# Kernel optimization log

Measured on AMD Instinct MI355X. Metric: run time of the kernel, lower is better.

The kernel has to match this reference:

```python
import jax, jax.numpy as jnp
import numpy as np

N = 100000      # nodes
E = 1600000     # edges
FX = 128        # raw node feature dim
MAXZ = 100      # z embedding / one-hot size
HID = 128       # hidden_channels
NL = 3          # num_layers
G = 512         # num graphs
BN_EPS = 1e-5


def _lin(key, din, dout):
    return jax.random.normal(key, (din, dout), jnp.float32) * (1.0 / np.sqrt(din))


def setup_inputs() -> dict:
    key = jax.random.key(0)
    ks = jax.random.split(key, 64)
    d = {}
    d["x"] = jax.random.normal(ks[0], (N, FX), jnp.float32)
    d["z"] = jax.random.randint(ks[1], (N,), 0, MAXZ)
    d["edge_index"] = jax.random.randint(ks[2], (2, E), 0, N)
    d["batch"] = jnp.sort(jax.random.randint(ks[3], (N,), 0, G))
    in0 = FX + 2 * MAXZ  # z_emb concatenated twice (faithful to source)
    ki = 4
    for l in range(NL):
        din = in0 if l == 0 else HID
        d[f"W1_{l}"] = _lin(ks[ki], din, HID); ki += 1
        d[f"b1_{l}"] = jnp.zeros((HID,), jnp.float32)
        d[f"W2_{l}"] = _lin(ks[ki], HID, HID); ki += 1
        d[f"b2_{l}"] = jnp.zeros((HID,), jnp.float32)
        d[f"g_{l}"] = jnp.ones((HID,), jnp.float32)
        d[f"be_{l}"] = jnp.zeros((HID,), jnp.float32)
    d["Wl1"] = _lin(ks[ki], NL * HID, HID); ki += 1
    d["bl1"] = jnp.zeros((HID,), jnp.float32)
    d["Wl2"] = _lin(ks[ki], HID, 1); ki += 1
    d["bl2"] = jnp.zeros((1,), jnp.float32)
    return d


def _gin_layer(h, src, dst, W1, b1, W2, b2, g, be):
    # GINConv with eps=0: nn(x + sum_{j->i} x_j)
    agg = jax.ops.segment_sum(h[src], dst, num_segments=N)  # [N, d]
    m = h + agg
    m = jax.nn.relu(m @ W1 + b1)
    m = jax.nn.relu(m @ W2 + b2)
    # training-mode BatchNorm1d over node axis (biased variance)
    mu = m.mean(0)
    var = jnp.mean((m - mu) ** 2, axis=0)
    return (m - mu) * jax.lax.rsqrt(var + BN_EPS) * g + be


def reference(x, z, edge_index, batch,
              W1_0, b1_0, W2_0, b2_0, g_0, be_0,
              W1_1, b1_1, W2_1, b2_1, g_1, be_1,
              W1_2, b1_2, W2_2, b2_2, g_2, be_2,
              Wl1, bl1, Wl2, bl2):
    src, dst = edge_index[0], edge_index[1]
    z_emb = jax.nn.one_hot(z, MAXZ, dtype=jnp.float32)  # [N, MAXZ]
    h = jnp.concatenate([z_emb, x], axis=1)
    h = jnp.concatenate([z_emb, h], axis=1)  # faithful double concat -> [N, FX+2*MAXZ]
    params = [(W1_0, b1_0, W2_0, b2_0, g_0, be_0),
              (W1_1, b1_1, W2_1, b2_1, g_1, be_1),
              (W1_2, b1_2, W2_2, b2_2, g_2, be_2)]
    xs = []
    for p in params:
        h = _gin_layer(h, src, dst, *p)
        xs.append(h)
    hcat = jnp.concatenate(xs, axis=1)  # jumping knowledge: [N, NL*HID]
    # global_mean_pool over graph ids
    counts = jax.ops.segment_sum(jnp.ones((N,), jnp.float32), batch, num_segments=G)
    pooled = jax.ops.segment_sum(hcat, batch, num_segments=G) / jnp.maximum(counts, 1.0)[:, None]
    out = jax.nn.relu(pooled @ Wl1 + bl1)
    # dropout is identity in eval / reference mode
    out = out @ Wl2 + bl2  # [G, 1]
    return out
```

## Files before the change

kernel.cpp:

```cpp
#include <hip/hip_runtime.h>
#include <hip/hip_bf16.h>

#define NN 100000
#define NROWS_PAD 100032
#define EE 1600000
#define GG 512
#define SCAN_CHUNK 512
#define SCAN_BLOCKS ((NN + SCAN_CHUNK - 1) / SCAN_CHUNK)
#define NPB 256
#define NB  ((NN + NPB - 1) / NPB)
#define PCHUNK 4096
#define PBLOCKS ((EE + PCHUNK - 1) / PCHUNK)
static constexpr float BN_EPS = 1e-5f;

typedef _Float16 half8 __attribute__((ext_vector_type(8)));
typedef _Float16 half4 __attribute__((ext_vector_type(4)));
typedef float floatx4 __attribute__((ext_vector_type(4)));


__global__ __launch_bounds__(256) void k_bhist(const int* __restrict__ EI,
                                               int* __restrict__ bcount)
{
    __shared__ int h[NB];
    const int t = threadIdx.x;
    for (int i = t; i < NB; i += 256) h[i] = 0;
    __syncthreads();
    const int e0 = blockIdx.x * PCHUNK;
    const int e1 = (e0 + PCHUNK < EE) ? e0 + PCHUNK : EE;
    for (int e = e0 + t; e < e1; e += 256)
        atomicAdd(&h[EI[EE + e] >> 8], 1);
    __syncthreads();
    for (int i = t; i < NB; i += 256)
        if (h[i]) atomicAdd(&bcount[i], h[i]);
}

__global__ __launch_bounds__(512) void k_bscan(const int* __restrict__ bcount,
                                               int* __restrict__ bstart,
                                               int* __restrict__ bcursor)
{
    __shared__ int s[512];
    int t = threadIdx.x;
    int v = (t < NB) ? bcount[t] : 0;
    s[t] = v;
    __syncthreads();
    for (int off = 1; off < 512; off <<= 1) {
        int u = (t >= off) ? s[t - off] : 0;
        __syncthreads();
        s[t] += u;
        __syncthreads();
    }
    if (t < NB) { int ex = s[t] - v; bstart[t] = ex; bcursor[t] = ex; }
    if (t == 0) bstart[NB] = EE;
}

__global__ __launch_bounds__(256) void k_part(const int* __restrict__ EI,
                                              int* __restrict__ bcursor,
                                              int* __restrict__ ebuf)
{
    __shared__ int h[NB];
    __shared__ int cur[NB];
    const int t = threadIdx.x;
    for (int i = t; i < NB; i += 256) h[i] = 0;
    __syncthreads();
    const int e0 = blockIdx.x * PCHUNK;
    const int e1 = (e0 + PCHUNK < EE) ? e0 + PCHUNK : EE;
    for (int e = e0 + t; e < e1; e += 256)
        atomicAdd(&h[EI[EE + e] >> 8], 1);
    __syncthreads();
    for (int i = t; i < NB; i += 256)
        cur[i] = h[i] ? atomicAdd(&bcursor[i], h[i]) : 0;
    __syncthreads();
    for (int e = e0 + t; e < e1; e += 256) {
        int s = EI[e], d = EI[EE + e];
        int pos = atomicAdd(&cur[d >> 8], 1);
        ebuf[pos] = s | ((d & (NPB - 1)) << 17);
    }
}

__global__ __launch_bounds__(256) void k_nhist(const int* __restrict__ ebuf,
                                               const int* __restrict__ bstart,
                                               int* __restrict__ hist)
{
    __shared__ int cnt[NPB];
    const int b = blockIdx.x, t = threadIdx.x;
    cnt[t] = 0;
    __syncthreads();
    const int e0 = bstart[b], e1 = bstart[b + 1];
    for (int e = e0 + t; e < e1; e += 256) {
        unsigned p = (unsigned)__builtin_nontemporal_load(&ebuf[e]);
        atomicAdd(&cnt[p >> 17], 1);
    }
    __syncthreads();
    int idx = b * NPB + t;
    if (idx < NN) hist[idx] = cnt[t];
}

__global__ __launch_bounds__(256) void k_scan1(const int* __restrict__ hist,
                                               int* __restrict__ partials)
{
    __shared__ int red[256];
    int b = blockIdx.x, t = threadIdx.x;
    int i0 = b * SCAN_CHUNK + 2 * t;
    int e0 = (i0 < NN) ? hist[i0] : 0;
    int e1 = (i0 + 1 < NN) ? hist[i0 + 1] : 0;
    red[t] = e0 + e1;
    __syncthreads();
    for (int off = 128; off > 0; off >>= 1) {
        if (t < off) red[t] += red[t + off];
        __syncthreads();
    }
    if (t == 0) partials[b] = red[0];
}

__global__ __launch_bounds__(256) void k_scan2(const int* __restrict__ partials,
                                               int* __restrict__ poffs,
                                               int* __restrict__ row_start)
{
    __shared__ int s[256];
    int t = threadIdx.x;
    int v = (t < SCAN_BLOCKS) ? partials[t] : 0;
    s[t] = v;
    __syncthreads();
    for (int off = 1; off < 256; off <<= 1) {
        int u = (t >= off) ? s[t - off] : 0;
        __syncthreads();
        s[t] += u;
        __syncthreads();
    }
    if (t < SCAN_BLOCKS) poffs[t] = s[t] - v;
    if (t == 0) row_start[NN] = EE;
}

__global__ __launch_bounds__(256) void k_scan3(const int* __restrict__ hist,
                                               const int* __restrict__ poffs,
                                               int* __restrict__ row_start)
{
    __shared__ int s[256];
    int b = blockIdx.x, t = threadIdx.x;
    int i0 = b * SCAN_CHUNK + 2 * t;
    int e0 = (i0 < NN) ? hist[i0] : 0;
    int e1 = (i0 + 1 < NN) ? hist[i0 + 1] : 0;
    int pair = e0 + e1;
    s[t] = pair;
    __syncthreads();
    for (int off = 1; off < 256; off <<= 1) {
        int u = (t >= off) ? s[t - off] : 0;
        __syncthreads();
        s[t] += u;
        __syncthreads();
    }
    int base = poffs[b] + s[t] - pair;
    if (i0 < NN)     row_start[i0] = base;
    if (i0 + 1 < NN) row_start[i0 + 1] = base + e0;
}

__global__ __launch_bounds__(256) void k_fill2(const int* __restrict__ ebuf,
                                               const int* __restrict__ bstart,
                                               const int* __restrict__ row_start,
                                               int* __restrict__ ssrc)
{
    __shared__ int cur[NPB];
    const int b = blockIdx.x, t = threadIdx.x;
    int idx = b * NPB + t;
    cur[t] = (idx < NN) ? row_start[idx] : 0;
    __syncthreads();
    const int e0 = bstart[b], e1 = bstart[b + 1];
    for (int e = e0 + t; e < e1; e += 256) {
        unsigned p = (unsigned)__builtin_nontemporal_load(&ebuf[e]);
        int pos = atomicAdd(&cur[p >> 17], 1);
        ssrc[pos] = (int)(p & 0x1FFFFu);
    }
}


__global__ __launch_bounds__(256) void k_xcast(const float* __restrict__ X,
                                               _Float16* __restrict__ Xh)
{
    int idx = blockIdx.x * 256 + threadIdx.x;
    const float4* src = (const float4*)X;
    float4 a = src[idx * 2], b = src[idx * 2 + 1];
    half8 o = { (_Float16)a.x, (_Float16)a.y, (_Float16)a.z, (_Float16)a.w,
                (_Float16)b.x, (_Float16)b.y, (_Float16)b.z, (_Float16)b.w };
    *(half8*)&Xh[idx * 8] = o;
}

__global__ __launch_bounds__(256) void k_prep(
    const float* __restrict__ W1, const float* __restrict__ W2,
    const float* __restrict__ scale, const float* __restrict__ shift,
    _Float16* __restrict__ Wt1, _Float16* __restrict__ Wt2,
    float* __restrict__ cvec, int l)
{
    int b = blockIdx.x, t = threadIdx.x;
    if (b < 64) {
        int idx = b * 256 + t;
        int n = idx >> 7, k = idx & 127;
        Wt1[idx] = (l == 0) ? (_Float16)W1[(200 + k) * 128 + n]
                            : (_Float16)(scale[k] * W1[k * 128 + n]);
    } else if (b < 128) {
        int idx = (b - 64) * 256 + t;
        int n = idx >> 7, k = idx & 127;
        Wt2[idx] = (_Float16)W2[k * 128 + n];
    } else if (t < 128) {
        float acc = 0.f;
        if (l != 0)
            for (int k = 0; k < 128; ++k) acc = fmaf(shift[k], W1[k * 128 + t], acc);
        cvec[t] = acc;
    }
}


#define MM_PREAMBLE(Wth)                                                     \
    __shared__ _Float16 Wl[128][136];                                        \
    const int tid = threadIdx.x;                                             \
    const int row0 = blockIdx.x * 64;                                        \
    {                                                                        \
        for (int it = 0; it < 8; ++it) {                                     \
            int idx = tid + it * 256;                                        \
            int r = idx >> 4, seg = idx & 15;                                \
            *(half8*)&Wl[r][seg * 8] = *(const half8*)&Wth[r * 128 + seg * 8];\
        }                                                                    \
    }

#define MM_CORE(Ah)                                                          \
    const int lane = tid & 63;                                               \
    const int wv = tid >> 6;                                                 \
    const int ml = lane & 15;                                                \
    const int quad = lane >> 4;                                              \
    const int wr = wv >> 1, wc = wv & 1;                                     \
    floatx4 acc[2][4];                                                       \
    for (int r = 0; r < 2; ++r)                                              \
        for (int t = 0; t < 4; ++t)                                          \
            acc[r][t] = (floatx4){0.f, 0.f, 0.f, 0.f};                       \
    {                                                                        \
        const size_t ar0 = (size_t)(row0 + 32 * wr + ml) * 128;              \
        const size_t ar1 = ar0 + (size_t)16 * 128;                           \
        _Pragma("unroll")                                                    \
        for (int kq = 0; kq < 4; ++kq) {                                     \
            int k0 = kq * 32;                                                \
            half8 a0 = *(const half8*)&Ah[ar0 + k0 + quad * 8];              \
            half8 a1 = *(const half8*)&Ah[ar1 + k0 + quad * 8];              \
            _Pragma("unroll")                                                \
            for (int t = 0; t < 4; ++t) {                                    \
                half8 bf = *(const half8*)&Wl[64 * wc + 16 * t + ml][k0 + quad * 8]; \
                acc[0][t] = __builtin_amdgcn_mfma_f32_16x16x32_f16(a0, bf, acc[0][t], 0, 0, 0); \
                acc[1][t] = __builtin_amdgcn_mfma_f32_16x16x32_f16(a1, bf, acc[1][t], 0, 0, 0); \
            }                                                                \
        }                                                                    \
    }

__global__ __launch_bounds__(256) void k_mm_embed(
    const _Float16* __restrict__ Ah, const _Float16* __restrict__ Wth,
    const int* __restrict__ Z, const float* __restrict__ W1,
    _Float16* __restrict__ Ph)
{
    MM_PREAMBLE(Wth)
    __syncthreads();
    MM_CORE(Ah)
    #pragma unroll
    for (int r = 0; r < 2; ++r)
        #pragma unroll
        for (int j = 0; j < 4; ++j) {
            int grow = row0 + 32 * wr + 16 * r + quad * 4 + j;
            if (grow < NN) {
                int zv = Z[grow];
                const float* w0 = &W1[zv * 128];
                const float* w1 = &W1[(100 + zv) * 128];
                #pragma unroll
                for (int t = 0; t < 4; ++t) {
                    int gcol = 64 * wc + 16 * t + ml;
                    float v = acc[r][t][j] + w0[gcol] + w1[gcol];
                    Ph[(size_t)grow * 128 + gcol] = (_Float16)v;
                }
            }
        }
}

__global__ __launch_bounds__(256) void k_mm1(
    const _Float16* __restrict__ Ah, const _Float16* __restrict__ Wth,
    _Float16* __restrict__ Ph)
{
    MM_PREAMBLE(Wth)
    __syncthreads();
    MM_CORE(Ah)
    #pragma unroll
    for (int r = 0; r < 2; ++r)
        #pragma unroll
        for (int j = 0; j < 4; ++j) {
            int grow = row0 + 32 * wr + 16 * r + quad * 4 + j;
            if (grow < NN) {
                #pragma unroll
                for (int t = 0; t < 4; ++t) {
                    int gcol = 64 * wc + 16 * t + ml;
                    Ph[(size_t)grow * 128 + gcol] = (_Float16)acc[r][t][j];
                }
            }
        }
}

__global__ __launch_bounds__(256) void k_mm2(
    const _Float16* __restrict__ Ah, const _Float16* __restrict__ Wth,
    const float* __restrict__ b2, _Float16* __restrict__ Oh,
    float* __restrict__ colsum, float* __restrict__ colsq)
{
    __shared__ float cs[128];
    __shared__ float cq[128];
    MM_PREAMBLE(Wth)
    if (tid < 128) { cs[tid] = 0.f; cq[tid] = 0.f; }
    __syncthreads();
    MM_CORE(Ah)
    float b2v[4];
    #pragma unroll
    for (int t = 0; t < 4; ++t) b2v[t] = b2[64 * wc + 16 * t + ml];
    float st[4] = {0.f, 0.f, 0.f, 0.f};
    float qt[4] = {0.f, 0.f, 0.f, 0.f};
    #pragma unroll
    for (int r = 0; r < 2; ++r)
        #pragma unroll
        for (int j = 0; j < 4; ++j) {
            int grow = row0 + 32 * wr + 16 * r + quad * 4 + j;
            if (grow < NN) {
                #pragma unroll
                for (int t = 0; t < 4; ++t) {
                    int gcol = 64 * wc + 16 * t + ml;
                    float v = fmaxf(acc[r][t][j] + b2v[t], 0.f);
                    Oh[(size_t)grow * 128 + gcol] = (_Float16)v;
                    st[t] += v;
                    qt[t] += v * v;
                }
            }
        }
    #pragma unroll
    for (int t = 0; t < 4; ++t) {
        int gcol = 64 * wc + 16 * t + ml;
        atomicAdd(&cs[gcol], st[t]);
        atomicAdd(&cq[gcol], qt[t]);
    }
    __syncthreads();
    if (tid < 128) {
        atomicAdd(&colsum[tid], cs[tid]);
        atomicAdd(&colsq[tid], cq[tid]);
    }
}


__global__ __launch_bounds__(256) void k_aggregate(
    const _Float16* __restrict__ Ph, const int* __restrict__ row_start,
    const int* __restrict__ ssrc, const float* __restrict__ b1,
    const float* __restrict__ cvec, _Float16* __restrict__ Mh)
{
    int idx = blockIdx.x * 256 + threadIdx.x;
    int node = idx >> 4, q = idx & 15;
    if (node >= NN) return;
    int s0 = row_start[node], s1 = row_start[node + 1];
    float degp1 = (float)(s1 - s0 + 1);
    float acc[8];
    half8 pv = *(const half8*)&Ph[(size_t)node * 128 + q * 8];
    #pragma unroll
    for (int j = 0; j < 8; ++j)
        acc[j] = (float)pv[j] + fmaf(degp1, cvec[q * 8 + j], b1[q * 8 + j]);
    int e = s0;
    for (; e + 3 < s1; e += 4) {
        int sa = __builtin_nontemporal_load(&ssrc[e]);
        int sb = __builtin_nontemporal_load(&ssrc[e + 1]);
        int sc = __builtin_nontemporal_load(&ssrc[e + 2]);
        int sd = __builtin_nontemporal_load(&ssrc[e + 3]);
        half8 va = *(const half8*)&Ph[(size_t)sa * 128 + q * 8];
        half8 vb = *(const half8*)&Ph[(size_t)sb * 128 + q * 8];
        half8 vc = *(const half8*)&Ph[(size_t)sc * 128 + q * 8];
        half8 vd = *(const half8*)&Ph[(size_t)sd * 128 + q * 8];
        #pragma unroll
        for (int j = 0; j < 8; ++j)
            acc[j] += ((float)va[j] + (float)vb[j]) + ((float)vc[j] + (float)vd[j]);
    }
    for (; e < s1; ++e) {
        int sa = __builtin_nontemporal_load(&ssrc[e]);
        half8 va = *(const half8*)&Ph[(size_t)sa * 128 + q * 8];
        #pragma unroll
        for (int j = 0; j < 8; ++j) acc[j] += (float)va[j];
    }
    half8 o;
    #pragma unroll
    for (int j = 0; j < 8; ++j) o[j] = (_Float16)fmaxf(acc[j], 0.f);
    __builtin_nontemporal_store(o, (half8*)&Mh[(size_t)node * 128 + q * 8]);
}

__global__ void k_bnfin(const float* __restrict__ colsum, const float* __restrict__ colsq,
                        const float* __restrict__ g, const float* __restrict__ be,
                        float* __restrict__ scale, float* __restrict__ shift)
{
    int c = threadIdx.x;
    float inv_n = 1.0f / (float)NN;
    float mu = colsum[c] * inv_n;
    float var = colsq[c] * inv_n - mu * mu;
    float sc = g[c] * rsqrtf(var + BN_EPS);
    scale[c] = sc;
    shift[c] = be[c] - mu * sc;
}

__global__ __launch_bounds__(128) void k_pool(
    const _Float16* __restrict__ Ah, const int* __restrict__ batch,
    const float* __restrict__ scale, const float* __restrict__ shift,
    float* __restrict__ pooled, int loff)
{
    __shared__ float red[8][128];
    int g = blockIdx.x;
    int t = threadIdx.x;
    int rg = t >> 4, seg = t & 15;
    int lo = 0, hi = NN;
    while (lo < hi) { int mid = (lo + hi) >> 1; if (batch[mid] < g) lo = mid + 1; else hi = mid; }
    int s = lo;
    lo = s; hi = NN;
    while (lo < hi) { int mid = (lo + hi) >> 1; if (batch[mid] < g + 1) lo = mid + 1; else hi = mid; }
    int e = lo;
    float acc[8] = {};
    for (int i = s + rg; i < e; i += 8) {
        half8 v = *(const half8*)&Ah[(size_t)i * 128 + seg * 8];
        #pragma unroll
        for (int j = 0; j < 8; ++j) acc[j] += (float)v[j];
    }
    #pragma unroll
    for (int j = 0; j < 8; ++j) red[rg][seg * 8 + j] = acc[j];
    __syncthreads();
    int cnt = e - s;
    float inv = 1.0f / (float)(cnt > 0 ? cnt : 1);
    if (t < 128) {
        float s_ = 0.f;
        #pragma unroll
        for (int r = 0; r < 8; ++r) s_ += red[r][t];
        pooled[g * 384 + loff + t] = fmaf(scale[t], s_ * inv, shift[t]);
    }
}

__global__ __launch_bounds__(128) void k_final(
    const float* __restrict__ pooled,
    const float* __restrict__ Wl1, const float* __restrict__ bl1,
    const float* __restrict__ Wl2, const float* __restrict__ bl2,
    float* __restrict__ out)
{
    __shared__ float pr[384];
    __shared__ float red[128];
    int g = blockIdx.x, j = threadIdx.x;
    for (int i = j; i < 384; i += 128) pr[i] = pooled[g * 384 + i];
    __syncthreads();
    float acc = bl1[j];
    for (int k = 0; k < 384; ++k) acc = fmaf(pr[k], Wl1[k * 128 + j], acc);
    float r = fmaxf(acc, 0.f) * Wl2[j];
    red[j] = r;
    __syncthreads();
    for (int off = 64; off > 0; off >>= 1) {
        if (j < off) red[j] += red[j + off];
        __syncthreads();
    }
    if (j == 0) out[g] = red[0] + bl2[0];
}

extern "C" void kernel_launch(void* const* d_in, const int* in_sizes, int n_in,
                              void* d_out, int out_size, void* d_ws, size_t ws_size,
                              hipStream_t stream)
{
    const float* x     = (const float*)d_in[0];
    const int*   z     = (const int*)d_in[1];
    const int*   ei    = (const int*)d_in[2];
    const int*   batch = (const int*)d_in[3];
    const float* W1a[3] = {(const float*)d_in[4],  (const float*)d_in[10], (const float*)d_in[16]};
    const float* b1a[3] = {(const float*)d_in[5],  (const float*)d_in[11], (const float*)d_in[17]};
    const float* W2a[3] = {(const float*)d_in[6],  (const float*)d_in[12], (const float*)d_in[18]};
    const float* b2a[3] = {(const float*)d_in[7],  (const float*)d_in[13], (const float*)d_in[19]};
    const float* ga[3]  = {(const float*)d_in[8],  (const float*)d_in[14], (const float*)d_in[20]};
    const float* bea[3] = {(const float*)d_in[9],  (const float*)d_in[15], (const float*)d_in[21]};
    const float* Wl1 = (const float*)d_in[22];
    const float* bl1 = (const float*)d_in[23];
    const float* Wl2 = (const float*)d_in[24];
    const float* bl2 = (const float*)d_in[25];
    float* out = (float*)d_out;

    char* ws = (char*)d_ws;
    size_t off = 0;
    auto alloc = [&](size_t bytes) {
        void* p = ws + off;
        off += (bytes + 255) & ~(size_t)255;
        return p;
    };
    _Float16* Xh  = (_Float16*)alloc((size_t)NROWS_PAD * 128 * 2);
    _Float16* Ph  = (_Float16*)alloc((size_t)NROWS_PAD * 128 * 2);
    _Float16* Mh  = (_Float16*)alloc((size_t)NROWS_PAD * 128 * 2);
    _Float16* Ahb = (_Float16*)alloc((size_t)NROWS_PAD * 128 * 2);
    _Float16* Wt1 = (_Float16*)alloc((size_t)128 * 128 * 2);
    _Float16* Wt2 = (_Float16*)alloc((size_t)128 * 128 * 2);
    int*   ebuf     = (int*)alloc((size_t)EE * 4);
    int*   ssrc     = (int*)alloc((size_t)EE * 4);
    int*   hist     = (int*)alloc((size_t)NN * 4);
    int*   row_st   = (int*)alloc((size_t)(NN + 1) * 4);
    int*   bcount   = (int*)alloc((size_t)NB * 4);
    int*   bstart   = (int*)alloc((size_t)(NB + 1) * 4);
    int*   bcursor  = (int*)alloc((size_t)NB * 4);
    int*   partials = (int*)alloc((size_t)SCAN_BLOCKS * 4);
    int*   poffs    = (int*)alloc((size_t)SCAN_BLOCKS * 4);
    float* cvec     = (float*)alloc(128 * 4);
    float* stats    = (float*)alloc(3 * 256 * 4);
    float* scale    = (float*)alloc(128 * 4);
    float* shift    = (float*)alloc(128 * 4);
    float* pooled   = (float*)alloc((size_t)GG * 384 * 4);

    const int gemmBlocks = (NN + 63) / 64;
    const int aggBlocks  = (NN * 16 + 255) / 256;

    hipMemsetAsync(stats, 0, 3 * 256 * 4, stream);
    hipMemsetAsync(bcount, 0, (size_t)NB * 4, stream);
    k_xcast<<<(NN * 128 / 8 + 255) / 256, 256, 0, stream>>>(x, Xh);
    k_bhist<<<PBLOCKS, 256, 0, stream>>>(ei, bcount);
    k_bscan<<<1, 512, 0, stream>>>(bcount, bstart, bcursor);
    k_part<<<PBLOCKS, 256, 0, stream>>>(ei, bcursor, ebuf);
    k_nhist<<<NB, 256, 0, stream>>>(ebuf, bstart, hist);
    k_scan1<<<SCAN_BLOCKS, 256, 0, stream>>>(hist, partials);
    k_scan2<<<1, 256, 0, stream>>>(partials, poffs, row_st);
    k_scan3<<<SCAN_BLOCKS, 256, 0, stream>>>(hist, poffs, row_st);
    k_fill2<<<NB, 256, 0, stream>>>(ebuf, bstart, row_st, ssrc);

    for (int l = 0; l < 3; ++l) {
        float* colsum = stats + l * 256;
        float* colsq  = stats + l * 256 + 128;
        k_prep<<<129, 256, 0, stream>>>(W1a[l], W2a[l], scale, shift, Wt1, Wt2, cvec, l);
        if (l == 0)
            k_mm_embed<<<gemmBlocks, 256, 0, stream>>>(Xh, Wt1, z, W1a[0], Ph);
        else
            k_mm1<<<gemmBlocks, 256, 0, stream>>>(Ahb, Wt1, Ph);
        k_aggregate<<<aggBlocks, 256, 0, stream>>>(Ph, row_st, ssrc, b1a[l], cvec, Mh);
        k_mm2<<<gemmBlocks, 256, 0, stream>>>(Mh, Wt2, b2a[l], Ahb, colsum, colsq);
        k_bnfin<<<1, 128, 0, stream>>>(colsum, colsq, ga[l], bea[l], scale, shift);
        k_pool<<<GG, 128, 0, stream>>>(Ahb, batch, scale, shift, pooled, l * 128);
    }
    k_final<<<GG, 128, 0, stream>>>(pooled, Wl1, bl1, Wl2, bl2, out);
}
```

Before: 713.5 us.

## Fuse neighbor aggregation into second GEMM and fold BN finalize into consumers

Merges the per-node sparse aggregation with the second MFMA GEMM, so aggregated rows go to LDS instead of a global Mh buffer. The separate BN-finalize kernel is removed and scale/shift are recomputed inline in k_prep and k_pool from the column sums. GEMM weight tiles are now read straight from global memory instead of being staged in LDS. This drops one full N×128 fp16 write and read plus two launches per layer. The cost is that the gather now uses 4 threads per node instead of 16, each holding 32 accumulators, which lowers memory-level parallelism and raises register pressure.

```diff
diff --git a/kernel.cpp b/kernel.cpp
--- a/kernel.cpp
+++ b/kernel.cpp
@@ -14,7 +14,6 @@
 static constexpr float BN_EPS = 1e-5f;
 
 typedef _Float16 half8 __attribute__((ext_vector_type(8)));
-typedef _Float16 half4 __attribute__((ext_vector_type(4)));
 typedef float floatx4 __attribute__((ext_vector_type(4)));
 
 
@@ -184,9 +183,21 @@
     *(half8*)&Xh[idx * 8] = o;
 }
 
+__device__ __forceinline__ void bn_sc_sh(const float* colsum, const float* colsq,
+                                         const float* g, const float* be, int k,
+                                         float& sc, float& sh)
+{
+    float inv_n = 1.0f / (float)NN;
+    float mu = colsum[k] * inv_n;
+    float var = colsq[k] * inv_n - mu * mu;
+    sc = g[k] * rsqrtf(var + BN_EPS);
+    sh = be[k] - mu * sc;
+}
+
 __global__ __launch_bounds__(256) void k_prep(
     const float* __restrict__ W1, const float* __restrict__ W2,
-    const float* __restrict__ scale, const float* __restrict__ shift,
+    const float* __restrict__ colsum, const float* __restrict__ colsq,
+    const float* __restrict__ g, const float* __restrict__ be,
     _Float16* __restrict__ Wt1, _Float16* __restrict__ Wt2,
     float* __restrict__ cvec, int l)
 {
@@ -194,34 +205,32 @@
     if (b < 64) {
         int idx = b * 256 + t;
         int n = idx >> 7, k = idx & 127;
-        Wt1[idx] = (l == 0) ? (_Float16)W1[(200 + k) * 128 + n]
-                            : (_Float16)(scale[k] * W1[k * 128 + n]);
+        if (l == 0) {
+            Wt1[idx] = (_Float16)W1[(200 + k) * 128 + n];
+        } else {
+            float sc, sh;
+            bn_sc_sh(colsum, colsq, g, be, k, sc, sh);
+            Wt1[idx] = (_Float16)(sc * W1[k * 128 + n]);
+        }
     } else if (b < 128) {
         int idx = (b - 64) * 256 + t;
         int n = idx >> 7, k = idx & 127;
         Wt2[idx] = (_Float16)W2[k * 128 + n];
     } else if (t < 128) {
         float acc = 0.f;
-        if (l != 0)
-            for (int k = 0; k < 128; ++k) acc = fmaf(shift[k], W1[k * 128 + t], acc);
+        if (l != 0) {
+            for (int k = 0; k < 128; ++k) {
+                float sc, sh;
+                bn_sc_sh(colsum, colsq, g, be, k, sc, sh);
+                acc = fmaf(sh, W1[k * 128 + t], acc);
+            }
+        }
         cvec[t] = acc;
     }
 }
 
 
-#define MM_PREAMBLE(Wth)                                                     \
-    __shared__ _Float16 Wl[128][136];                                        \
-    const int tid = threadIdx.x;                                             \
-    const int row0 = blockIdx.x * 64;                                        \
-    {                                                                        \
-        for (int it = 0; it < 8; ++it) {                                     \
-            int idx = tid + it * 256;                                        \
-            int r = idx >> 4, seg = idx & 15;                                \
-            *(half8*)&Wl[r][seg * 8] = *(const half8*)&Wth[r * 128 + seg * 8];\
-        }                                                                    \
-    }
-
-#define MM_CORE(Ah)                                                          \
+#define MM_CORE_G(Ah, Wth)                                                   \
     const int lane = tid & 63;                                               \
     const int wv = tid >> 6;                                                 \
     const int ml = lane & 15;                                                \
@@ -241,7 +250,7 @@
             half8 a1 = *(const half8*)&Ah[ar1 + k0 + quad * 8];              \
             _Pragma("unroll")                                                \
             for (int t = 0; t < 4; ++t) {                                    \
-                half8 bf = *(const half8*)&Wl[64 * wc + 16 * t + ml][k0 + quad * 8]; \
+                half8 bf = *(const half8*)&Wth[(size_t)(64 * wc + 16 * t + ml) * 128 + k0 + quad * 8]; \
                 acc[0][t] = __builtin_amdgcn_mfma_f32_16x16x32_f16(a0, bf, acc[0][t], 0, 0, 0); \
                 acc[1][t] = __builtin_amdgcn_mfma_f32_16x16x32_f16(a1, bf, acc[1][t], 0, 0, 0); \
             }                                                                \
@@ -253,9 +262,9 @@
     const int* __restrict__ Z, const float* __restrict__ W1,
     _Float16* __restrict__ Ph)
 {
-    MM_PREAMBLE(Wth)
-    __syncthreads();
-    MM_CORE(Ah)
+    const int tid = threadIdx.x;
+    const int row0 = blockIdx.x * 64;
+    MM_CORE_G(Ah, Wth)
     #pragma unroll
     for (int r = 0; r < 2; ++r)
         #pragma unroll
@@ -279,9 +288,9 @@
     const _Float16* __restrict__ Ah, const _Float16* __restrict__ Wth,
     _Float16* __restrict__ Ph)
 {
-    MM_PREAMBLE(Wth)
-    __syncthreads();
-    MM_CORE(Ah)
+    const int tid = threadIdx.x;
+    const int row0 = blockIdx.x * 64;
+    MM_CORE_G(Ah, Wth)
     #pragma unroll
     for (int r = 0; r < 2; ++r)
         #pragma unroll
@@ -297,17 +306,106 @@
         }
 }
 
-__global__ __launch_bounds__(256) void k_mm2(
-    const _Float16* __restrict__ Ah, const _Float16* __restrict__ Wth,
+
+__global__ __launch_bounds__(256) void k_aggmm2(
+    const _Float16* __restrict__ Ph, const int* __restrict__ row_start,
+    const int* __restrict__ ssrc, const float* __restrict__ b1,
+    const float* __restrict__ cvec, const _Float16* __restrict__ Wt2,
     const float* __restrict__ b2, _Float16* __restrict__ Oh,
     float* __restrict__ colsum, float* __restrict__ colsq)
 {
+    __shared__ _Float16 Mt[64][130];
     __shared__ float cs[128];
     __shared__ float cq[128];
-    MM_PREAMBLE(Wth)
+    const int tid = threadIdx.x;
+    const int row0 = blockIdx.x * 64;
+
+    {
+        const int nrow = tid >> 2;
+        const int node = row0 + nrow;
+        const int c0 = (tid & 3) * 32;
+        float ga[32];
+        if (node < NN) {
+            int s0 = row_start[node], s1 = row_start[node + 1];
+            float degp1 = (float)(s1 - s0 + 1);
+            #pragma unroll
+            for (int c = 0; c < 4; ++c) {
+                half8 pv = *(const half8*)&Ph[(size_t)node * 128 + c0 + c * 8];
+                #pragma unroll
+                for (int j = 0; j < 8; ++j)
+                    ga[c * 8 + j] = (float)pv[j]
+                        + fmaf(degp1, cvec[c0 + c * 8 + j], b1[c0 + c * 8 + j]);
+            }
+            int e = s0;
+            for (; e + 3 < s1; e += 4) {
+                int sa = __builtin_nontemporal_load(&ssrc[e]);
+                int sb = __builtin_nontemporal_load(&ssrc[e + 1]);
+                int sc_ = __builtin_nontemporal_load(&ssrc[e + 2]);
+                int sd = __builtin_nontemporal_load(&ssrc[e + 3]);
+                const _Float16* pa = &Ph[(size_t)sa * 128 + c0];
+                const _Float16* pb = &Ph[(size_t)sb * 128 + c0];
+                const _Float16* pc = &Ph[(size_t)sc_ * 128 + c0];
+                const _Float16* pd = &Ph[(size_t)sd * 128 + c0];
+                #pragma unroll
+                for (int c = 0; c < 4; ++c) {
+                    half8 va = *(const half8*)&pa[c * 8];
+                    half8 vb = *(const half8*)&pb[c * 8];
+                    half8 vc = *(const half8*)&pc[c * 8];
+                    half8 vd = *(const half8*)&pd[c * 8];
+                    #pragma unroll
+                    for (int j = 0; j < 8; ++j)
+                        ga[c * 8 + j] += ((float)va[j] + (float)vb[j])
+                                       + ((float)vc[j] + (float)vd[j]);
+                }
+            }
+            for (; e < s1; ++e) {
+                int sa = __builtin_nontemporal_load(&ssrc[e]);
+                const _Float16* pa = &Ph[(size_t)sa * 128 + c0];
+                #pragma unroll
+                for (int c = 0; c < 4; ++c) {
+                    half8 va = *(const half8*)&pa[c * 8];
+                    #pragma unroll
+                    for (int j = 0; j < 8; ++j) ga[c * 8 + j] += (float)va[j];
+                }
+            }
+            #pragma unroll
+            for (int c = 0; c < 4; ++c) {
+                half8 o;
+                #pragma unroll
+                for (int j = 0; j < 8; ++j) o[j] = (_Float16)fmaxf(ga[c * 8 + j], 0.f);
+                *(half8*)&Mt[nrow][c0 + c * 8] = o;
+            }
+        } else {
+            half8 zz = {};
+            #pragma unroll
+            for (int c = 0; c < 4; ++c) *(half8*)&Mt[nrow][c0 + c * 8] = zz;
+        }
+    }
     if (tid < 128) { cs[tid] = 0.f; cq[tid] = 0.f; }
     __syncthreads();
-    MM_CORE(Ah)
+
+    const int lane = tid & 63;
+    const int wv = tid >> 6;
+    const int ml = lane & 15;
+    const int quad = lane >> 4;
+    const int wr = wv >> 1, wc = wv & 1;
+    floatx4 acc[2][4];
+    #pragma unroll
+    for (int r = 0; r < 2; ++r)
+        #pragma unroll
+        for (int t = 0; t < 4; ++t) acc[r][t] = (floatx4){0.f, 0.f, 0.f, 0.f};
+    #pragma unroll
+    for (int kq = 0; kq < 4; ++kq) {
+        int k0 = kq * 32;
+        half8 a0 = *(const half8*)&Mt[32 * wr + ml][k0 + quad * 8];
+        half8 a1 = *(const half8*)&Mt[32 * wr + 16 + ml][k0 + quad * 8];
+        #pragma unroll
+        for (int t = 0; t < 4; ++t) {
+            half8 bf = *(const half8*)&Wt2[(size_t)(64 * wc + 16 * t + ml) * 128 + k0 + quad * 8];
+            acc[0][t] = __builtin_amdgcn_mfma_f32_16x16x32_f16(a0, bf, acc[0][t], 0, 0, 0);
+            acc[1][t] = __builtin_amdgcn_mfma_f32_16x16x32_f16(a1, bf, acc[1][t], 0, 0, 0);
+        }
+    }
     float b2v[4];
     #pragma unroll
     for (int t = 0; t < 4; ++t) b2v[t] = b2[64 * wc + 16 * t + ml];
@@ -343,63 +441,10 @@
 }
 
 
-__global__ __launch_bounds__(256) void k_aggregate(
-    const _Float16* __restrict__ Ph, const int* __restrict__ row_start,
-    const int* __restrict__ ssrc, const float* __restrict__ b1,
-    const float* __restrict__ cvec, _Float16* __restrict__ Mh)
-{
-    int idx = blockIdx.x * 256 + threadIdx.x;
-    int node = idx >> 4, q = idx & 15;
-    if (node >= NN) return;
-    int s0 = row_start[node], s1 = row_start[node + 1];
-    float degp1 = (float)(s1 - s0 + 1);
-    float acc[8];
-    half8 pv = *(const half8*)&Ph[(size_t)node * 128 + q * 8];
-    #pragma unroll
-    for (int j = 0; j < 8; ++j)
-        acc[j] = (float)pv[j] + fmaf(degp1, cvec[q * 8 + j], b1[q * 8 + j]);
-    int e = s0;
-    for (; e + 3 < s1; e += 4) {
-        int sa = __builtin_nontemporal_load(&ssrc[e]);
-        int sb = __builtin_nontemporal_load(&ssrc[e + 1]);
-        int sc = __builtin_nontemporal_load(&ssrc[e + 2]);
-        int sd = __builtin_nontemporal_load(&ssrc[e + 3]);
-        half8 va = *(const half8*)&Ph[(size_t)sa * 128 + q * 8];
-        half8 vb = *(const half8*)&Ph[(size_t)sb * 128 + q * 8];
-        half8 vc = *(const half8*)&Ph[(size_t)sc * 128 + q * 8];
-        half8 vd = *(const half8*)&Ph[(size_t)sd * 128 + q * 8];
-        #pragma unroll
-        for (int j = 0; j < 8; ++j)
-            acc[j] += ((float)va[j] + (float)vb[j]) + ((float)vc[j] + (float)vd[j]);
-    }
-    for (; e < s1; ++e) {
-        int sa = __builtin_nontemporal_load(&ssrc[e]);
-        half8 va = *(const half8*)&Ph[(size_t)sa * 128 + q * 8];
-        #pragma unroll
-        for (int j = 0; j < 8; ++j) acc[j] += (float)va[j];
-    }
-    half8 o;
-    #pragma unroll
-    for (int j = 0; j < 8; ++j) o[j] = (_Float16)fmaxf(acc[j], 0.f);
-    __builtin_nontemporal_store(o, (half8*)&Mh[(size_t)node * 128 + q * 8]);
-}
-
-__global__ void k_bnfin(const float* __restrict__ colsum, const float* __restrict__ colsq,
-                        const float* __restrict__ g, const float* __restrict__ be,
-                        float* __restrict__ scale, float* __restrict__ shift)
-{
-    int c = threadIdx.x;
-    float inv_n = 1.0f / (float)NN;
-    float mu = colsum[c] * inv_n;
-    float var = colsq[c] * inv_n - mu * mu;
-    float sc = g[c] * rsqrtf(var + BN_EPS);
-    scale[c] = sc;
-    shift[c] = be[c] - mu * sc;
-}
-
 __global__ __launch_bounds__(128) void k_pool(
     const _Float16* __restrict__ Ah, const int* __restrict__ batch,
-    const float* __restrict__ scale, const float* __restrict__ shift,
+    const float* __restrict__ colsum, const float* __restrict__ colsq,
+    const float* __restrict__ g_, const float* __restrict__ be,
     float* __restrict__ pooled, int loff)
 {
     __shared__ float red[8][128];
@@ -427,7 +472,9 @@
         float s_ = 0.f;
         #pragma unroll
         for (int r = 0; r < 8; ++r) s_ += red[r][t];
-        pooled[g * 384 + loff + t] = fmaf(scale[t], s_ * inv, shift[t]);
+        float sc, sh;
+        bn_sc_sh(colsum, colsq, g_, be, t, sc, sh);
+        pooled[g * 384 + loff + t] = fmaf(sc, s_ * inv, sh);
     }
 }
 
@@ -483,7 +530,6 @@
     };
     _Float16* Xh  = (_Float16*)alloc((size_t)NROWS_PAD * 128 * 2);
     _Float16* Ph  = (_Float16*)alloc((size_t)NROWS_PAD * 128 * 2);
-    _Float16* Mh  = (_Float16*)alloc((size_t)NROWS_PAD * 128 * 2);
     _Float16* Ahb = (_Float16*)alloc((size_t)NROWS_PAD * 128 * 2);
     _Float16* Wt1 = (_Float16*)alloc((size_t)128 * 128 * 2);
     _Float16* Wt2 = (_Float16*)alloc((size_t)128 * 128 * 2);
@@ -498,12 +544,9 @@
     int*   poffs    = (int*)alloc((size_t)SCAN_BLOCKS * 4);
     float* cvec     = (float*)alloc(128 * 4);
     float* stats    = (float*)alloc(3 * 256 * 4);
-    float* scale    = (float*)alloc(128 * 4);
-    float* shift    = (float*)alloc(128 * 4);
     float* pooled   = (float*)alloc((size_t)GG * 384 * 4);
 
     const int gemmBlocks = (NN + 63) / 64;
-    const int aggBlocks  = (NN * 16 + 255) / 256;
 
     hipMemsetAsync(stats, 0, 3 * 256 * 4, stream);
     hipMemsetAsync(bcount, 0, (size_t)NB * 4, stream);
@@ -520,15 +563,20 @@
     for (int l = 0; l < 3; ++l) {
         float* colsum = stats + l * 256;
         float* colsq  = stats + l * 256 + 128;
-        k_prep<<<129, 256, 0, stream>>>(W1a[l], W2a[l], scale, shift, Wt1, Wt2, cvec, l);
+        const float* psum = (l > 0) ? stats + (l - 1) * 256 : stats;
+        const float* psq  = (l > 0) ? stats + (l - 1) * 256 + 128 : stats + 128;
+        const float* pg   = (l > 0) ? ga[l - 1] : ga[0];
+        const float* pbe  = (l > 0) ? bea[l - 1] : bea[0];
+        k_prep<<<129, 256, 0, stream>>>(W1a[l], W2a[l], psum, psq, pg, pbe,
+                                        Wt1, Wt2, cvec, l);
         if (l == 0)
             k_mm_embed<<<gemmBlocks, 256, 0, stream>>>(Xh, Wt1, z, W1a[0], Ph);
         else
             k_mm1<<<gemmBlocks, 256, 0, stream>>>(Ahb, Wt1, Ph);
-        k_aggregate<<<aggBlocks, 256, 0, stream>>>(Ph, row_st, ssrc, b1a[l], cvec, Mh);
-        k_mm2<<<gemmBlocks, 256, 0, stream>>>(Mh, Wt2, b2a[l], Ahb, colsum, colsq);
-        k_bnfin<<<1, 128, 0, stream>>>(colsum, colsq, ga[l], bea[l], scale, shift);
-        k_pool<<<GG, 128, 0, stream>>>(Ahb, batch, scale, shift, pooled, l * 128);
+        k_aggmm2<<<gemmBlocks, 256, 0, stream>>>(Ph, row_st, ssrc, b1a[l], cvec,
+                                                 Wt2, b2a[l], Ahb, colsum, colsq);
+        k_pool<<<GG, 128, 0, stream>>>(Ahb, batch, colsum, colsq, ga[l], bea[l],
+                                       pooled, l * 128);
     }
     k_final<<<GG, 128, 0, stream>>>(pooled, Wl1, bl1, Wl2, bl2, out);
 }
```

Result: slower. 823.3 us (+15.4%).
